# Performance work log

Hardware: AMD Instinct MI355X
Metric: run time of the kernel (lower is better)

## Reference

```python
import jax, jax.numpy as jnp
import numpy as np

N_SLOTS, SLOT_DIM, FEAT_DIM, N_HEADS = 8, 256, 128, 4
HEAD_DIM = SLOT_DIM // N_HEADS
B, H, W = 32, 64, 64


def layernorm(x, g, b, eps=1e-5):
    mu = jnp.mean(x, axis=-1, keepdims=True)
    var = jnp.var(x, axis=-1, keepdims=True)
    return (x - mu) * jax.lax.rsqrt(var + eps) * g + b


def setup_inputs() -> dict:
    key = jax.random.key(0)
    ks = jax.random.split(key, 20)
    s = lambda i, shape, sc: (jax.random.normal(ks[i], shape, dtype=jnp.float32) * sc)
    return {
        'features': s(0, (B, FEAT_DIM, H, W), 1.0),
        'slots': s(1, (B, N_SLOTS, SLOT_DIM), 1.0),
        'Wq': s(2, (SLOT_DIM, SLOT_DIM), 0.05), 'bq': jnp.zeros((SLOT_DIM,), jnp.float32),
        'Wk': s(3, (FEAT_DIM, SLOT_DIM), 0.05), 'bk': jnp.zeros((SLOT_DIM,), jnp.float32),
        'Wv': s(4, (FEAT_DIM, SLOT_DIM), 0.05), 'bv': jnp.zeros((SLOT_DIM,), jnp.float32),
        'W_ih': s(5, (3 * SLOT_DIM, SLOT_DIM), 0.05), 'b_ih': jnp.zeros((3 * SLOT_DIM,), jnp.float32),
        'W_hh': s(6, (3 * SLOT_DIM, SLOT_DIM), 0.05), 'b_hh': jnp.zeros((3 * SLOT_DIM,), jnp.float32),
        'g_pre': jnp.ones((SLOT_DIM,), jnp.float32), 'b_pre': jnp.zeros((SLOT_DIM,), jnp.float32),
        'g_post': jnp.ones((SLOT_DIM,), jnp.float32), 'b_post': jnp.zeros((SLOT_DIM,), jnp.float32),
        'W1': s(7, (SLOT_DIM, 2 * SLOT_DIM), 0.05), 'b1': jnp.zeros((2 * SLOT_DIM,), jnp.float32),
        'W2': s(8, (2 * SLOT_DIM, SLOT_DIM), 0.05), 'b2': jnp.zeros((SLOT_DIM,), jnp.float32),
    }


def reference(features, slots, Wq, bq, Wk, bk, Wv, bv, W_ih, b_ih, W_hh, b_hh,
              g_pre, b_pre, g_post, b_post, W1, b1, W2, b2):
    b, c, h, w = features.shape
    n = h * w
    feats = features.transpose(0, 2, 3, 1).reshape(b, n, c)  # (B, HW, C)

    slots_n = layernorm(slots, g_pre, b_pre)
    q = (slots_n @ Wq + bq).reshape(b, N_SLOTS, N_HEADS, HEAD_DIM)
    k = (feats @ Wk + bk).reshape(b, n, N_HEADS, HEAD_DIM)
    v = (feats @ Wv + bv).reshape(b, n, N_HEADS, HEAD_DIM)

    scale = HEAD_DIM ** -0.5
    # scores: (B, heads, slots, HW); softmax over the SLOT axis (competition)
    scores = jnp.einsum('bshd,bnhd->bhsn', q, k) * scale
    attn = jax.nn.softmax(scores, axis=2)
    agg = jnp.einsum('bhsn,bnhd->bshd', attn, v).reshape(b, N_SLOTS, SLOT_DIM)

    # GRUCell (torch semantics): gates ordered r, z, n
    x = agg.reshape(b * N_SLOTS, SLOT_DIM)
    hprev = slots.reshape(b * N_SLOTS, SLOT_DIM)
    gi = x @ W_ih.T + b_ih
    gh = hprev @ W_hh.T + b_hh
    i_r, i_z, i_n = jnp.split(gi, 3, axis=-1)
    h_r, h_z, h_n = jnp.split(gh, 3, axis=-1)
    r = jax.nn.sigmoid(i_r + h_r)
    z = jax.nn.sigmoid(i_z + h_z)
    nn_ = jnp.tanh(i_n + r * h_n)
    hnew = (1.0 - z) * nn_ + z * hprev
    updated = hnew.reshape(b, N_SLOTS, SLOT_DIM)

    # post-norm + MLP residual (dropout is identity in eval)
    refined = jax.nn.relu(layernorm(updated, g_post, b_post) @ W1 + b1) @ W2 + b2
    return updated + refined
```

## Files before the change

kernel.cpp:

```cpp
#include <hip/hip_runtime.h>
#include <hip/hip_bf16.h>

#define NSLOT 8
#define SDIM 256
#define FDIM 128
#define NHEAD 4
#define HDIM 64
#define NPOS 4096

typedef short v8s __attribute__((ext_vector_type(8)));
typedef short v4s __attribute__((ext_vector_type(4)));
typedef float v4f __attribute__((ext_vector_type(4)));

__device__ __forceinline__ unsigned short f2bf(float x) {
    __hip_bfloat16 h = __float2bfloat16(x);
    unsigned short u; __builtin_memcpy(&u, &h, 2); return u;
}
__device__ __forceinline__ float bfr2f(unsigned short u) {
    __hip_bfloat16 h; __builtin_memcpy(&h, &u, 2); return __bfloat162float(h);
}
__device__ __forceinline__ void splitf(float x, unsigned short& hi, unsigned short& lo) {
    hi = f2bf(x);
    lo = f2bf(x - bfr2f(hi));
}

__global__ __launch_bounds__(256) void k_prep(
    const float* __restrict__ slots,
    const float* __restrict__ Wq, const float* __restrict__ bq,
    const float* __restrict__ g_pre, const float* __restrict__ b_pre,
    const float* __restrict__ Wk, const float* __restrict__ bk,
    const float* __restrict__ W1, const float* __restrict__ W2,
    const float* __restrict__ W_ih, const float* __restrict__ W_hh,
    const float* __restrict__ Wv,
    unsigned short* __restrict__ qkT_ws, float* __restrict__ qb_ws,
    unsigned short* __restrict__ W1Th, unsigned short* __restrict__ W1Tl,
    unsigned short* __restrict__ W2Th, unsigned short* __restrict__ W2Tl,
    unsigned short* __restrict__ WihH, unsigned short* __restrict__ WihL,
    unsigned short* __restrict__ WhhH, unsigned short* __restrict__ WhhL,
    unsigned short* __restrict__ WvTH, unsigned short* __restrict__ WvTl,
    float* __restrict__ agg_ws)
{
    int blk = blockIdx.x, t = threadIdx.x;
    __shared__ __align__(16) float s_ln[256];
    __shared__ __align__(16) float q_l[256];
    __shared__ float r1[4], r2[4];
    __shared__ float tl[32][33];

    if (blk >= 560) {
        int id3 = blk - 560;
        int k0 = (id3 & 3) * 32, n0 = (id3 >> 2) * 32;
        for (int i = 0; i < 4; i++) {
            int idx = i * 256 + t, r = idx >> 5, c = idx & 31;
            tl[r][c] = Wv[(size_t)(k0 + r) * 256 + n0 + c];
        }
        __syncthreads();
        for (int i = 0; i < 4; i++) {
            int idx = i * 256 + t, r = idx >> 5, c = idx & 31;
            unsigned short hi, lo; splitf(tl[c][r], hi, lo);
            WvTH[(size_t)(n0 + r) * 128 + k0 + c] = hi;
            WvTl[(size_t)(n0 + r) * 128 + k0 + c] = lo;
        }
        return;
    }
    if (blk >= 512) {
        int id2 = blk - 512;
        const float* src; unsigned short *dh, *dl; int r0;
        if (id2 < 24) { src = W_ih; dh = WihH; dl = WihL; r0 = id2 * 32; }
        else          { src = W_hh; dh = WhhH; dl = WhhL; r0 = (id2 - 24) * 32; }
        for (int i = 0; i < 32; i++) {
            size_t idx = (size_t)(r0 + i) * 256 + t;
            unsigned short hi, lo; splitf(src[idx], hi, lo);
            dh[idx] = hi; dl[idx] = lo;
        }
        return;
    }
    if (blk >= 256) {
        int id = blk - 256;
        const float* src; unsigned short *dh, *dl; int N, K, k0, n0;
        if (id < 128) { src = W1; dh = W1Th; dl = W1Tl; N = 512; K = 256;
                        k0 = (id >> 4) * 32; n0 = (id & 15) * 32; }
        else          { int i2 = id - 128; src = W2; dh = W2Th; dl = W2Tl; N = 256; K = 512;
                        k0 = (i2 >> 3) * 32; n0 = (i2 & 7) * 32; }
        for (int i = 0; i < 4; i++) {
            int idx = i * 256 + t, r = idx >> 5, c = idx & 31;
            tl[r][c] = src[(size_t)(k0 + r) * N + n0 + c];
        }
        __syncthreads();
        for (int i = 0; i < 4; i++) {
            int idx = i * 256 + t, r = idx >> 5, c = idx & 31;
            unsigned short hi, lo; splitf(tl[c][r], hi, lo);
            dh[(size_t)(n0 + r) * K + k0 + c] = hi;
            dl[(size_t)(n0 + r) * K + k0 + c] = lo;
        }
        return;
    }

    int b = blk >> 3, s = blk & 7;
    if (s == 0)
        for (int i = 0; i < 8; i++) agg_ws[b * 2048 + i * 256 + t] = 0.0f;

    float x = slots[(size_t)(b * 8 + s) * 256 + t];
    float sum = x, sq = x * x;
    #pragma unroll
    for (int m = 1; m <= 32; m <<= 1) {
        sum += __shfl_xor(sum, m, 64);
        sq  += __shfl_xor(sq, m, 64);
    }
    int w = t >> 6, lane = t & 63;
    if (lane == 0) { r1[w] = sum; r2[w] = sq; }
    __syncthreads();
    sum = r1[0] + r1[1] + r1[2] + r1[3];
    sq  = r2[0] + r2[1] + r2[2] + r2[3];
    float mu  = sum * (1.0f / 256);
    float var = sq * (1.0f / 256) - mu * mu;
    float rstd = rsqrtf(var + 1e-5f);
    s_ln[t] = (x - mu) * rstd * g_pre[t] + b_pre[t];
    __syncthreads();

    float qacc = bq[t];
    for (int k = 0; k < 256; k += 4) {
        float4 l4 = *(const float4*)&s_ln[k];
        qacc += l4.x * Wq[(k + 0) * 256 + t]
              + l4.y * Wq[(k + 1) * 256 + t]
              + l4.z * Wq[(k + 2) * 256 + t]
              + l4.w * Wq[(k + 3) * 256 + t];
    }
    q_l[t] = qacc;
    __syncthreads();

    int c = t & 127, h0 = t >> 7;
    #pragma unroll
    for (int hi_ = 0; hi_ < 2; hi_++) {
        int hh = h0 + hi_ * 2;
        const float4* wk4 = (const float4*)&Wk[(size_t)c * 256 + hh * 64];
        const float4* q4  = (const float4*)&q_l[hh * 64];
        float acc = 0.0f;
        #pragma unroll
        for (int d4 = 0; d4 < 16; d4++) {
            float4 wv = wk4[d4]; float4 qv = q4[d4];
            acc += wv.x * qv.x + wv.y * qv.y + wv.z * qv.z + wv.w * qv.w;
        }
        qkT_ws[(size_t)(b * 32 + hh * 8 + s) * 128 + c] = f2bf(acc);
    }
    if (t < 4) {
        float acc = 0.0f;
        for (int d = 0; d < 64; d++)
            acc += bk[t * 64 + d] * q_l[t * 64 + d];
        qb_ws[b * 32 + t * 8 + s] = acc;
    }
}

__global__ __launch_bounds__(256, 4) void k_attn(
    const float* __restrict__ feat,
    const unsigned short* __restrict__ WvTH, const unsigned short* __restrict__ WvTl,
    const float* __restrict__ bv,
    const unsigned short* __restrict__ qkT, const float* __restrict__ qb_ws,
    float* __restrict__ agg_ws)
{
    __shared__ __align__(16) char smem[31360];
    unsigned short* featPC = (unsigned short*)smem;
    unsigned short* featCP = (unsigned short*)(smem + 8704);
    unsigned short* attFH  = (unsigned short*)smem;
    unsigned short* attFL  = (unsigned short*)(smem + 8704);
    float*          s_attn = (float*)(smem + 23040);
    unsigned short* s_aT   = (unsigned short*)(smem + 27648);
    float*          s_S    = (float*)(smem + 31232);

    int t = threadIdx.x, b = blockIdx.y, n0 = blockIdx.x * 128;
    int wv_ = t >> 6, lane = t & 63, quad = lane >> 4, l16 = lane & 15;
    int mt = wv_ >> 1, nt = wv_ & 1;
    int sp  = l16 + mt * 16;
    int shs = l16 + nt * 16;

    v8s bq_[4];
    #pragma unroll
    for (int ch = 0; ch < 4; ch++)
        bq_[ch] = *(const v8s*)&qkT[(b * 32 + shs) * 128 + ch * 32 + quad * 8];
    float qbv = qb_ws[b * 32 + shs];
    if (t < 32) s_S[t] = 0.0f;

    v4f accF[4];
    #pragma unroll
    for (int i = 0; i < 4; i++) accF[i] = (v4f){0.f, 0.f, 0.f, 0.f};

    int c0 = (t >> 3) * 4, p0 = (t & 7) * 4;
    size_t fbase = (size_t)b * (FDIM * NPOS);

    float fv[4][4];
    #pragma unroll
    for (int r = 0; r < 4; r++) {
        float4 f = *(const float4*)&feat[fbase + (size_t)(c0 + r) * NPOS + n0 + p0];
        fv[r][0] = f.x; fv[r][1] = f.y; fv[r][2] = f.z; fv[r][3] = f.w;
    }

    #pragma unroll
    for (int tt = 0; tt < 4; ++tt) {
        __syncthreads();
        unsigned short us[4][4];
        #pragma unroll
        for (int r = 0; r < 4; r++)
            #pragma unroll
            for (int j = 0; j < 4; j++) us[r][j] = f2bf(fv[r][j]);
        #pragma unroll
        for (int r = 0; r < 4; r++)
            *(v4s*)&featCP[(c0 + r) * 56 + p0] =
                (v4s){(short)us[r][0], (short)us[r][1], (short)us[r][2], (short)us[r][3]};
        #pragma unroll
        for (int j = 0; j < 4; j++)
            *(v4s*)&featPC[(p0 + j) * 136 + c0] =
                (v4s){(short)us[0][j], (short)us[1][j], (short)us[2][j], (short)us[3][j]};
        __syncthreads();

        if (tt < 3) {
            #pragma unroll
            for (int r = 0; r < 4; r++) {
                float4 f = *(const float4*)&feat[fbase + (size_t)(c0 + r) * NPOS
                                                 + n0 + (tt + 1) * 32 + p0];
                fv[r][0] = f.x; fv[r][1] = f.y; fv[r][2] = f.z; fv[r][3] = f.w;
            }
        }

        v4f acc = (v4f){0.f, 0.f, 0.f, 0.f};
        #pragma unroll
        for (int ch = 0; ch < 4; ch++) {
            v8s a = *(const v8s*)&featPC[sp * 136 + ch * 32 + quad * 8];
            acc = __builtin_amdgcn_mfma_f32_16x16x32_bf16(a, bq_[ch], acc, 0, 0, 0);
        }
        int pb = mt * 16 + quad * 4;
        #pragma unroll
        for (int r = 0; r < 4; r++)
            s_attn[(pb + r) * 36 + shs] = (acc[r] + qbv) * 0.125f;
        __syncthreads();

        if (t < 128) {
            int p = t >> 2, h2 = t & 3;
            float* a = &s_attn[p * 36 + h2 * 8];
            float m = a[0];
            for (int s = 1; s < 8; s++) m = fmaxf(m, a[s]);
            float e[8], ssum = 0.0f;
            for (int s = 0; s < 8; s++) { e[s] = __expf(a[s] - m); ssum += e[s]; }
            float inv = 1.0f / ssum;
            float sv[8];
            #pragma unroll
            for (int s = 0; s < 8; s++) {
                sv[s] = e[s] * inv;
                s_aT[(h2 * 8 + s) * 56 + p] = f2bf(sv[s]);
            }
            #pragma unroll
            for (int mm = 4; mm <= 32; mm <<= 1)
                #pragma unroll
                for (int s = 0; s < 8; s++) sv[s] += __shfl_xor(sv[s], mm, 64);
            if ((t & 63) < 4)
                #pragma unroll
                for (int s = 0; s < 8; s++) atomicAdd(&s_S[h2 * 8 + s], sv[s]);
        }
        __syncthreads();

        v8s aA0 = *(const v8s*)&s_aT[l16 * 56 + quad * 8];
        v8s aA1 = *(const v8s*)&s_aT[(l16 + 16) * 56 + quad * 8];
        v8s bF0 = *(const v8s*)&featCP[(l16 + wv_ * 32) * 56 + quad * 8];
        v8s bF1 = *(const v8s*)&featCP[(l16 + wv_ * 32 + 16) * 56 + quad * 8];
        accF[0] = __builtin_amdgcn_mfma_f32_16x16x32_bf16(aA0, bF0, accF[0], 0, 0, 0);
        accF[1] = __builtin_amdgcn_mfma_f32_16x16x32_bf16(aA0, bF1, accF[1], 0, 0, 0);
        accF[2] = __builtin_amdgcn_mfma_f32_16x16x32_bf16(aA1, bF0, accF[2], 0, 0, 0);
        accF[3] = __builtin_amdgcn_mfma_f32_16x16x32_bf16(aA1, bF1, accF[3], 0, 0, 0);
    }
    __syncthreads();
    #pragma unroll
    for (int mt2 = 0; mt2 < 2; mt2++)
        #pragma unroll
        for (int ntl = 0; ntl < 2; ntl++) {
            v4f f = accF[mt2 * 2 + ntl];
            int cc = wv_ * 32 + ntl * 16 + l16;
            #pragma unroll
            for (int r = 0; r < 4; r++) {
                unsigned short hi, lo; splitf(f[r], hi, lo);
                attFH[(mt2 * 16 + quad * 4 + r) * 136 + cc] = hi;
                attFL[(mt2 * 16 + quad * 4 + r) * 136 + cc] = lo;
            }
        }
    __syncthreads();

    int h = wv_;
    int am = h * 8 + (l16 & 7);
    for (int nt2 = 0; nt2 < 4; nt2++) {
        int n = h * 64 + nt2 * 16 + l16;
        v4f acc = (v4f){0.f, 0.f, 0.f, 0.f};
        #pragma unroll
        for (int kk = 0; kk < 4; kk++) {
            int ko = kk * 32 + quad * 8;
            v8s ah = *(const v8s*)&attFH[am * 136 + ko];
            v8s al = *(const v8s*)&attFL[am * 136 + ko];
            v8s bh = *(const v8s*)&WvTH[(size_t)n * 128 + ko];
            v8s bl = *(const v8s*)&WvTl[(size_t)n * 128 + ko];
            acc = __builtin_amdgcn_mfma_f32_16x16x32_bf16(al, bh, acc, 0, 0, 0);
            acc = __builtin_amdgcn_mfma_f32_16x16x32_bf16(ah, bl, acc, 0, 0, 0);
            acc = __builtin_amdgcn_mfma_f32_16x16x32_bf16(ah, bh, acc, 0, 0, 0);
        }
        float bvn = bv[n];
        if (quad < 2) {
            #pragma unroll
            for (int r = 0; r < 4; r++) {
                int s = quad * 4 + r;
                atomicAdd(&agg_ws[b * 2048 + s * 256 + n],
                          acc[r] + s_S[h * 8 + s] * bvn);
            }
        }
    }
}

__global__ __launch_bounds__(256) void k_gate(
    const float* __restrict__ agg, const float* __restrict__ slots,
    const unsigned short* __restrict__ WihH, const unsigned short* __restrict__ WihL,
    const float* __restrict__ b_ih,
    const unsigned short* __restrict__ WhhH, const unsigned short* __restrict__ WhhL,
    const float* __restrict__ b_hh,
    float* __restrict__ G)
{
    int ntile = blockIdx.x, mtile = blockIdx.y, t = threadIdx.x;
    bool hhalf = ntile >= 12;
    int jbase = (hhalf ? ntile - 12 : ntile) * 64;
    const float* X = hhalf ? slots : agg;
    const unsigned short* BH = hhalf ? WhhH : WihH;
    const unsigned short* BL = hhalf ? WhhL : WihL;
    const float* bias = hhalf ? b_hh : b_ih;
    int gofs = hhalf ? 768 : 0;
    int m0 = mtile * 16;

    __shared__ __align__(16) unsigned short aH[16][264];
    __shared__ __align__(16) unsigned short aL[16][264];
    for (int i = 0; i < 4; i++) {
        int idx = i * 256 + t;
        int r = idx >> 6, q = idx & 63;
        float4 f = *(const float4*)&X[(size_t)(m0 + r) * 256 + q * 4];
        unsigned short h0,l0,h1,l1,h2,l2,h3,l3;
        splitf(f.x, h0, l0); splitf(f.y, h1, l1);
        splitf(f.z, h2, l2); splitf(f.w, h3, l3);
        *(v4s*)&aH[r][q * 4] = (v4s){(short)h0,(short)h1,(short)h2,(short)h3};
        *(v4s*)&aL[r][q * 4] = (v4s){(short)l0,(short)l1,(short)l2,(short)l3};
    }
    __syncthreads();

    int w = t >> 6, lane = t & 63, quad = lane >> 4, l16 = lane & 15;
    int jrow = jbase + w * 16 + l16;
    v4f acc = (v4f){0.f, 0.f, 0.f, 0.f};
    #pragma unroll
    for (int kk = 0; kk < 8; kk++) {
        int ko = kk * 32 + quad * 8;
        v8s ah = *(const v8s*)&aH[l16][ko];
        v8s al = *(const v8s*)&aL[l16][ko];
        v8s bh = *(const v8s*)&BH[(size_t)jrow * 256 + ko];
        v8s bl = *(const v8s*)&BL[(size_t)jrow * 256 + ko];
        acc = __builtin_amdgcn_mfma_f32_16x16x32_bf16(al, bh, acc, 0, 0, 0);
        acc = __builtin_amdgcn_mfma_f32_16x16x32_bf16(ah, bl, acc, 0, 0, 0);
        acc = __builtin_amdgcn_mfma_f32_16x16x32_bf16(ah, bh, acc, 0, 0, 0);
    }
    float bv_ = bias[jrow];
    int gj = gofs + jbase + w * 16 + l16;
    #pragma unroll
    for (int r = 0; r < 4; r++)
        G[(size_t)(m0 + quad * 4 + r) * 1536 + gj] = acc[r] + bv_;
}

__device__ __forceinline__ float gru1(float ir, float iz, float in_,
                                      float hr, float hz, float hn, float hp) {
    float r = 1.0f / (1.0f + __expf(-(ir + hr)));
    float z = 1.0f / (1.0f + __expf(-(iz + hz)));
    float n = tanhf(in_ + r * hn);
    return (1.0f - z) * n + z * hp;
}

__global__ __launch_bounds__(1024) void k_tail2(
    const float* __restrict__ slots, const float* __restrict__ G,
    const float* __restrict__ g_post, const float* __restrict__ b_post,
    const unsigned short* __restrict__ W1Th, const unsigned short* __restrict__ W1Tl,
    const float* __restrict__ b1,
    const unsigned short* __restrict__ W2Th, const unsigned short* __restrict__ W2Tl,
    const float* __restrict__ b2,
    float* __restrict__ hnF, float* __restrict__ out)
{
    __shared__ __align__(16) char smem[50176];
    unsigned short* lnH   = (unsigned short*)smem;
    unsigned short* lnLo  = (unsigned short*)(smem + 8448);
    unsigned short* y1H   = (unsigned short*)(smem + 16896);
    unsigned short* y1Lo  = (unsigned short*)(smem + 33536);

    int t = threadIdx.x, m0 = blockIdx.x * 16;
    int w = t >> 6, lane = t & 63, quad = lane >> 4, l16 = lane & 15;

    {
        int row = m0 + w, c0 = lane * 4;
        const float* gp = &G[(size_t)row * 1536 + c0];
        float4 gir = *(const float4*)(gp);
        float4 giz = *(const float4*)(gp + 256);
        float4 gin = *(const float4*)(gp + 512);
        float4 ghr = *(const float4*)(gp + 768);
        float4 ghz = *(const float4*)(gp + 1024);
        float4 ghn = *(const float4*)(gp + 1280);
        float4 hp  = *(const float4*)&slots[(size_t)row * 256 + c0];
        float h0 = gru1(gir.x, giz.x, gin.x, ghr.x, ghz.x, ghn.x, hp.x);
        float h1 = gru1(gir.y, giz.y, gin.y, ghr.y, ghz.y, ghn.y, hp.y);
        float h2 = gru1(gir.z, giz.z, gin.z, ghr.z, ghz.z, ghn.z, hp.z);
        float h3 = gru1(gir.w, giz.w, gin.w, ghr.w, ghz.w, ghn.w, hp.w);
        float ssum = h0 + h1 + h2 + h3;
        float ssq  = h0*h0 + h1*h1 + h2*h2 + h3*h3;
        #pragma unroll
        for (int m = 1; m <= 32; m <<= 1) {
            ssum += __shfl_xor(ssum, m, 64);
            ssq  += __shfl_xor(ssq, m, 64);
        }
        float mu = ssum * (1.0f / 256);
        float var = ssq * (1.0f / 256) - mu * mu;
        float rstd = rsqrtf(var + 1e-5f);
        float4 gp4 = *(const float4*)&g_post[c0];
        float4 bp4 = *(const float4*)&b_post[c0];
        float l0 = (h0 - mu) * rstd * gp4.x + bp4.x;
        float l1 = (h1 - mu) * rstd * gp4.y + bp4.y;
        float l2 = (h2 - mu) * rstd * gp4.z + bp4.z;
        float l3 = (h3 - mu) * rstd * gp4.w + bp4.w;
        unsigned short a0,c0s,a1,c1s,a2,c2s,a3,c3s;
        splitf(l0, a0, c0s); splitf(l1, a1, c1s);
        splitf(l2, a2, c2s); splitf(l3, a3, c3s);
        *(v4s*)&lnH[w * 264 + c0]  = (v4s){(short)a0,(short)a1,(short)a2,(short)a3};
        *(v4s*)&lnLo[w * 264 + c0] = (v4s){(short)c0s,(short)c1s,(short)c2s,(short)c3s};
        float4 hv4; hv4.x = h0; hv4.y = h1; hv4.z = h2; hv4.w = h3;
        *(float4*)&hnF[(size_t)row * 256 + c0] = hv4;
    }
    __syncthreads();

    #pragma unroll
    for (int i = 0; i < 2; i++) {
        int ntile = w * 2 + i;
        int n = ntile * 16 + l16;
        v4f acc = (v4f){0.f, 0.f, 0.f, 0.f};
        #pragma unroll
        for (int kk = 0; kk < 8; kk++) {
            int ko = kk * 32 + quad * 8;
            v8s ah = *(const v8s*)&lnH[l16 * 264 + ko];
            v8s al = *(const v8s*)&lnLo[l16 * 264 + ko];
            v8s bh = *(const v8s*)&W1Th[(size_t)n * 256 + ko];
            v8s bl = *(const v8s*)&W1Tl[(size_t)n * 256 + ko];
            acc = __builtin_amdgcn_mfma_f32_16x16x32_bf16(al, bh, acc, 0, 0, 0);
            acc = __builtin_amdgcn_mfma_f32_16x16x32_bf16(ah, bl, acc, 0, 0, 0);
            acc = __builtin_amdgcn_mfma_f32_16x16x32_bf16(ah, bh, acc, 0, 0, 0);
        }
        float bb = b1[n];
        #pragma unroll
        for (int r = 0; r < 4; r++) {
            float y = fmaxf(acc[r] + bb, 0.0f);
            unsigned short hi, lo; splitf(y, hi, lo);
            y1H[(quad * 4 + r) * 520 + n]  = hi;
            y1Lo[(quad * 4 + r) * 520 + n] = lo;
        }
    }
    __syncthreads();

    {
        int n = w * 16 + l16;
        v4f acc = (v4f){0.f, 0.f, 0.f, 0.f};
        #pragma unroll
        for (int kk = 0; kk < 16; kk++) {
            int ko = kk * 32 + quad * 8;
            v8s ah = *(const v8s*)&y1H[l16 * 520 + ko];
            v8s al = *(const v8s*)&y1Lo[l16 * 520 + ko];
            v8s bh = *(const v8s*)&W2Th[(size_t)n * 512 + ko];
            v8s bl = *(const v8s*)&W2Tl[(size_t)n * 512 + ko];
            acc = __builtin_amdgcn_mfma_f32_16x16x32_bf16(al, bh, acc, 0, 0, 0);
            acc = __builtin_amdgcn_mfma_f32_16x16x32_bf16(ah, bl, acc, 0, 0, 0);
            acc = __builtin_amdgcn_mfma_f32_16x16x32_bf16(ah, bh, acc, 0, 0, 0);
        }
        float bb = b2[n];
        #pragma unroll
        for (int r = 0; r < 4; r++) {
            int m = m0 + quad * 4 + r;
            out[(size_t)m * 256 + n] = hnF[(size_t)m * 256 + n] + acc[r] + bb;
        }
    }
}

extern "C" void kernel_launch(void* const* d_in, const int* in_sizes, int n_in,
                              void* d_out, int out_size, void* d_ws, size_t ws_size,
                              hipStream_t stream) {
    const float* features = (const float*)d_in[0];
    const float* slots    = (const float*)d_in[1];
    const float* Wq   = (const float*)d_in[2];
    const float* bq   = (const float*)d_in[3];
    const float* Wk   = (const float*)d_in[4];
    const float* bk   = (const float*)d_in[5];
    const float* Wv   = (const float*)d_in[6];
    const float* bv   = (const float*)d_in[7];
    const float* W_ih = (const float*)d_in[8];
    const float* b_ih = (const float*)d_in[9];
    const float* W_hh = (const float*)d_in[10];
    const float* b_hh = (const float*)d_in[11];
    const float* g_pre  = (const float*)d_in[12];
    const float* b_pre  = (const float*)d_in[13];
    const float* g_post = (const float*)d_in[14];
    const float* b_post = (const float*)d_in[15];
    const float* W1 = (const float*)d_in[16];
    const float* b1 = (const float*)d_in[17];
    const float* W2 = (const float*)d_in[18];
    const float* b2 = (const float*)d_in[19];
    float* out = (float*)d_out;

    char* wsb = (char*)d_ws;
    float* G               = (float*)wsb;
    unsigned short* qkT_ws = (unsigned short*)wsb;
    float* qb_ws           = (float*)(wsb + 262144);
    unsigned short* W1Th   = (unsigned short*)(wsb + 1572864);
    unsigned short* W1Tl   = (unsigned short*)(wsb + 1835008);
    unsigned short* W2Th   = (unsigned short*)(wsb + 2097152);
    unsigned short* W2Tl   = (unsigned short*)(wsb + 2359296);
    unsigned short* WihH   = (unsigned short*)(wsb + 2621440);
    unsigned short* WihL   = (unsigned short*)(wsb + 3014656);
    unsigned short* WhhH   = (unsigned short*)(wsb + 3407872);
    unsigned short* WhhL   = (unsigned short*)(wsb + 3801088);
    unsigned short* WvTH   = (unsigned short*)(wsb + 4194304);
    unsigned short* WvTl   = (unsigned short*)(wsb + 4259840);
    float* hnF             = (float*)(wsb + 4325376);
    float* agg_ws = out;

    k_prep<<<dim3(592), dim3(256), 0, stream>>>(
        slots, Wq, bq, g_pre, b_pre, Wk, bk, W1, W2, W_ih, W_hh, Wv,
        qkT_ws, qb_ws, W1Th, W1Tl, W2Th, W2Tl,
        WihH, WihL, WhhH, WhhL, WvTH, WvTl, agg_ws);
    k_attn<<<dim3(32, 32), dim3(256), 0, stream>>>(
        features, WvTH, WvTl, bv, qkT_ws, qb_ws, agg_ws);
    k_gate<<<dim3(24, 16), dim3(256), 0, stream>>>(
        agg_ws, slots, WihH, WihL, b_ih, WhhH, WhhL, b_hh, G);
    k_tail2<<<dim3(16), dim3(1024), 0, stream>>>(
        slots, G, g_post, b_post, W1Th, W1Tl, b1, W2Th, W2Tl, b2, hnF, out);
}
```

Before: 193.4 us.

## Replace MFMA tail MLP with fp32 vector kernel over more blocks

Replaces the split-bf16 MFMA tail kernel (16 blocks of 1024 threads) with a plain fp32 FMA kernel that handles 4 rows per 256-thread block across 64 blocks, reading W1/W2 directly. This removes the W1/W2 transpose-and-split blocks from the prep kernel and the hnF round-trip through global memory. The tail is spread over more CUs but does scalar FMAs and rereads the fp32 weights once per block.

Measured after the change: 218.4 us. 1.13x slower.

```diff
diff --git a/kernel.cpp b/kernel.cpp
--- a/kernel.cpp
+++ b/kernel.cpp
@@ -29,12 +29,9 @@
     const float* __restrict__ Wq, const float* __restrict__ bq,
     const float* __restrict__ g_pre, const float* __restrict__ b_pre,
     const float* __restrict__ Wk, const float* __restrict__ bk,
-    const float* __restrict__ W1, const float* __restrict__ W2,
     const float* __restrict__ W_ih, const float* __restrict__ W_hh,
     const float* __restrict__ Wv,
     unsigned short* __restrict__ qkT_ws, float* __restrict__ qb_ws,
-    unsigned short* __restrict__ W1Th, unsigned short* __restrict__ W1Tl,
-    unsigned short* __restrict__ W2Th, unsigned short* __restrict__ W2Tl,
     unsigned short* __restrict__ WihH, unsigned short* __restrict__ WihL,
     unsigned short* __restrict__ WhhH, unsigned short* __restrict__ WhhL,
     unsigned short* __restrict__ WvTH, unsigned short* __restrict__ WvTl,
@@ -46,8 +43,8 @@
     __shared__ float r1[4], r2[4];
     __shared__ float tl[32][33];
 
-    if (blk >= 560) {
-        int id3 = blk - 560;
+    if (blk >= 304) {
+        int id3 = blk - 304;
         int k0 = (id3 & 3) * 32, n0 = (id3 >> 2) * 32;
         for (int i = 0; i < 4; i++) {
             int idx = i * 256 + t, r = idx >> 5, c = idx & 31;
@@ -62,8 +59,8 @@
         }
         return;
     }
-    if (blk >= 512) {
-        int id2 = blk - 512;
+    if (blk >= 256) {
+        int id2 = blk - 256;
         const float* src; unsigned short *dh, *dl; int r0;
         if (id2 < 24) { src = W_ih; dh = WihH; dl = WihL; r0 = id2 * 32; }
         else          { src = W_hh; dh = WhhH; dl = WhhL; r0 = (id2 - 24) * 32; }
@@ -71,26 +68,6 @@
             size_t idx = (size_t)(r0 + i) * 256 + t;
             unsigned short hi, lo; splitf(src[idx], hi, lo);
             dh[idx] = hi; dl[idx] = lo;
-        }
-        return;
-    }
-    if (blk >= 256) {
-        int id = blk - 256;
-        const float* src; unsigned short *dh, *dl; int N, K, k0, n0;
-        if (id < 128) { src = W1; dh = W1Th; dl = W1Tl; N = 512; K = 256;
-                        k0 = (id >> 4) * 32; n0 = (id & 15) * 32; }
-        else          { int i2 = id - 128; src = W2; dh = W2Th; dl = W2Tl; N = 256; K = 512;
-                        k0 = (i2 >> 3) * 32; n0 = (i2 & 7) * 32; }
-        for (int i = 0; i < 4; i++) {
-            int idx = i * 256 + t, r = idx >> 5, c = idx & 31;
-            tl[r][c] = src[(size_t)(k0 + r) * N + n0 + c];
-        }
-        __syncthreads();
-        for (int i = 0; i < 4; i++) {
-            int idx = i * 256 + t, r = idx >> 5, c = idx & 31;
-            unsigned short hi, lo; splitf(tl[c][r], hi, lo);
-            dh[(size_t)(n0 + r) * K + k0 + c] = hi;
-            dl[(size_t)(n0 + r) * K + k0 + c] = lo;
         }
         return;
     }
@@ -370,111 +347,100 @@
     return (1.0f - z) * n + z * hp;
 }
 
-__global__ __launch_bounds__(1024) void k_tail2(
+__global__ __launch_bounds__(256) void k_tail_vec(
     const float* __restrict__ slots, const float* __restrict__ G,
     const float* __restrict__ g_post, const float* __restrict__ b_post,
-    const unsigned short* __restrict__ W1Th, const unsigned short* __restrict__ W1Tl,
-    const float* __restrict__ b1,
-    const unsigned short* __restrict__ W2Th, const unsigned short* __restrict__ W2Tl,
-    const float* __restrict__ b2,
-    float* __restrict__ hnF, float* __restrict__ out)
+    const float* __restrict__ W1, const float* __restrict__ b1,
+    const float* __restrict__ W2, const float* __restrict__ b2,
+    float* __restrict__ out)
 {
-    __shared__ __align__(16) char smem[50176];
-    unsigned short* lnH   = (unsigned short*)smem;
-    unsigned short* lnLo  = (unsigned short*)(smem + 8448);
-    unsigned short* y1H   = (unsigned short*)(smem + 16896);
-    unsigned short* y1Lo  = (unsigned short*)(smem + 33536);
-
-    int t = threadIdx.x, m0 = blockIdx.x * 16;
-    int w = t >> 6, lane = t & 63, quad = lane >> 4, l16 = lane & 15;
-
+    __shared__ __align__(16) float s_ln[4][260];
+    __shared__ __align__(16) float s_y1[4][516];
+    __shared__ float pS[4][4], pQ[4][4];
+
+    int t = threadIdx.x, m0 = blockIdx.x * 4;
+    int w = t >> 6, lane = t & 63;
+
+    float hnew[4];
+    #pragma unroll
+    for (int r = 0; r < 4; r++) {
+        int row = m0 + r;
+        const float* gp = &G[(size_t)row * 1536 + t];
+        float hp = slots[(size_t)row * 256 + t];
+        hnew[r] = gru1(gp[0], gp[256], gp[512], gp[768], gp[1024], gp[1280], hp);
+    }
+    float ps[4], pq[4];
+    #pragma unroll
+    for (int r = 0; r < 4; r++) { ps[r] = hnew[r]; pq[r] = hnew[r] * hnew[r]; }
+    #pragma unroll
+    for (int mm = 1; mm <= 32; mm <<= 1)
+        #pragma unroll
+        for (int r = 0; r < 4; r++) {
+            ps[r] += __shfl_xor(ps[r], mm, 64);
+            pq[r] += __shfl_xor(pq[r], mm, 64);
+        }
+    if (lane == 0)
+        #pragma unroll
+        for (int r = 0; r < 4; r++) { pS[r][w] = ps[r]; pQ[r][w] = pq[r]; }
+    __syncthreads();
     {
-        int row = m0 + w, c0 = lane * 4;
-        const float* gp = &G[(size_t)row * 1536 + c0];
-        float4 gir = *(const float4*)(gp);
-        float4 giz = *(const float4*)(gp + 256);
-        float4 gin = *(const float4*)(gp + 512);
-        float4 ghr = *(const float4*)(gp + 768);
-        float4 ghz = *(const float4*)(gp + 1024);
-        float4 ghn = *(const float4*)(gp + 1280);
-        float4 hp  = *(const float4*)&slots[(size_t)row * 256 + c0];
-        float h0 = gru1(gir.x, giz.x, gin.x, ghr.x, ghz.x, ghn.x, hp.x);
-        float h1 = gru1(gir.y, giz.y, gin.y, ghr.y, ghz.y, ghn.y, hp.y);
-        float h2 = gru1(gir.z, giz.z, gin.z, ghr.z, ghz.z, ghn.z, hp.z);
-        float h3 = gru1(gir.w, giz.w, gin.w, ghr.w, ghz.w, ghn.w, hp.w);
-        float ssum = h0 + h1 + h2 + h3;
-        float ssq  = h0*h0 + h1*h1 + h2*h2 + h3*h3;
-        #pragma unroll
-        for (int m = 1; m <= 32; m <<= 1) {
-            ssum += __shfl_xor(ssum, m, 64);
-            ssq  += __shfl_xor(ssq, m, 64);
-        }
-        float mu = ssum * (1.0f / 256);
-        float var = ssq * (1.0f / 256) - mu * mu;
-        float rstd = rsqrtf(var + 1e-5f);
-        float4 gp4 = *(const float4*)&g_post[c0];
-        float4 bp4 = *(const float4*)&b_post[c0];
-        float l0 = (h0 - mu) * rstd * gp4.x + bp4.x;
-        float l1 = (h1 - mu) * rstd * gp4.y + bp4.y;
-        float l2 = (h2 - mu) * rstd * gp4.z + bp4.z;
-        float l3 = (h3 - mu) * rstd * gp4.w + bp4.w;
-        unsigned short a0,c0s,a1,c1s,a2,c2s,a3,c3s;
-        splitf(l0, a0, c0s); splitf(l1, a1, c1s);
-        splitf(l2, a2, c2s); splitf(l3, a3, c3s);
-        *(v4s*)&lnH[w * 264 + c0]  = (v4s){(short)a0,(short)a1,(short)a2,(short)a3};
-        *(v4s*)&lnLo[w * 264 + c0] = (v4s){(short)c0s,(short)c1s,(short)c2s,(short)c3s};
-        float4 hv4; hv4.x = h0; hv4.y = h1; hv4.z = h2; hv4.w = h3;
-        *(float4*)&hnF[(size_t)row * 256 + c0] = hv4;
-    }
-    __syncthreads();
-
-    #pragma unroll
-    for (int i = 0; i < 2; i++) {
-        int ntile = w * 2 + i;
-        int n = ntile * 16 + l16;
-        v4f acc = (v4f){0.f, 0.f, 0.f, 0.f};
-        #pragma unroll
-        for (int kk = 0; kk < 8; kk++) {
-            int ko = kk * 32 + quad * 8;
-            v8s ah = *(const v8s*)&lnH[l16 * 264 + ko];
-            v8s al = *(const v8s*)&lnLo[l16 * 264 + ko];
-            v8s bh = *(const v8s*)&W1Th[(size_t)n * 256 + ko];
-            v8s bl = *(const v8s*)&W1Tl[(size_t)n * 256 + ko];
-            acc = __builtin_amdgcn_mfma_f32_16x16x32_bf16(al, bh, acc, 0, 0, 0);
-            acc = __builtin_amdgcn_mfma_f32_16x16x32_bf16(ah, bl, acc, 0, 0, 0);
-            acc = __builtin_amdgcn_mfma_f32_16x16x32_bf16(ah, bh, acc, 0, 0, 0);
-        }
-        float bb = b1[n];
+        float gpv = g_post[t], bpv = b_post[t];
         #pragma unroll
         for (int r = 0; r < 4; r++) {
-            float y = fmaxf(acc[r] + bb, 0.0f);
-            unsigned short hi, lo; splitf(y, hi, lo);
-            y1H[(quad * 4 + r) * 520 + n]  = hi;
-            y1Lo[(quad * 4 + r) * 520 + n] = lo;
-        }
-    }
-    __syncthreads();
-
+            float s = pS[r][0] + pS[r][1] + pS[r][2] + pS[r][3];
+            float q = pQ[r][0] + pQ[r][1] + pQ[r][2] + pQ[r][3];
+            float mu = s * (1.0f / 256);
+            float var = q * (1.0f / 256) - mu * mu;
+            float rstd = rsqrtf(var + 1e-5f);
+            s_ln[r][t] = (hnew[r] - mu) * rstd * gpv + bpv;
+        }
+    }
+    __syncthreads();
+
+    float a0[4] = {0.f, 0.f, 0.f, 0.f}, a1[4] = {0.f, 0.f, 0.f, 0.f};
+    #define MLP1_STEP(KK, COMP) { \
+        float wA = W1[(size_t)(k + KK) * 512 + t]; \
+        float wB = W1[(size_t)(k + KK) * 512 + t + 256]; \
+        a0[0] += l0.COMP * wA; a1[0] += l0.COMP * wB; \
+        a0[1] += l1.COMP * wA; a1[1] += l1.COMP * wB; \
+        a0[2] += l2.COMP * wA; a1[2] += l2.COMP * wB; \
+        a0[3] += l3.COMP * wA; a1[3] += l3.COMP * wB; }
+    for (int k = 0; k < 256; k += 4) {
+        float4 l0 = *(const float4*)&s_ln[0][k];
+        float4 l1 = *(const float4*)&s_ln[1][k];
+        float4 l2 = *(const float4*)&s_ln[2][k];
+        float4 l3 = *(const float4*)&s_ln[3][k];
+        MLP1_STEP(0, x) MLP1_STEP(1, y) MLP1_STEP(2, z) MLP1_STEP(3, w)
+    }
+    #undef MLP1_STEP
     {
-        int n = w * 16 + l16;
-        v4f acc = (v4f){0.f, 0.f, 0.f, 0.f};
-        #pragma unroll
-        for (int kk = 0; kk < 16; kk++) {
-            int ko = kk * 32 + quad * 8;
-            v8s ah = *(const v8s*)&y1H[l16 * 520 + ko];
-            v8s al = *(const v8s*)&y1Lo[l16 * 520 + ko];
-            v8s bh = *(const v8s*)&W2Th[(size_t)n * 512 + ko];
-            v8s bl = *(const v8s*)&W2Tl[(size_t)n * 512 + ko];
-            acc = __builtin_amdgcn_mfma_f32_16x16x32_bf16(al, bh, acc, 0, 0, 0);
-            acc = __builtin_amdgcn_mfma_f32_16x16x32_bf16(ah, bl, acc, 0, 0, 0);
-            acc = __builtin_amdgcn_mfma_f32_16x16x32_bf16(ah, bh, acc, 0, 0, 0);
-        }
-        float bb = b2[n];
+        float b1a = b1[t], b1b = b1[t + 256];
         #pragma unroll
         for (int r = 0; r < 4; r++) {
-            int m = m0 + quad * 4 + r;
-            out[(size_t)m * 256 + n] = hnF[(size_t)m * 256 + n] + acc[r] + bb;
-        }
+            s_y1[r][t]       = fmaxf(a0[r] + b1a, 0.0f);
+            s_y1[r][t + 256] = fmaxf(a1[r] + b1b, 0.0f);
+        }
+    }
+    __syncthreads();
+
+    float o[4] = {0.f, 0.f, 0.f, 0.f};
+    #define MLP2_STEP(KK, COMP) { \
+        float wv = W2[(size_t)(k + KK) * 256 + t]; \
+        o[0] += y0.COMP * wv; o[1] += y1v.COMP * wv; \
+        o[2] += y2.COMP * wv; o[3] += y3.COMP * wv; }
+    for (int k = 0; k < 512; k += 4) {
+        float4 y0  = *(const float4*)&s_y1[0][k];
+        float4 y1v = *(const float4*)&s_y1[1][k];
+        float4 y2  = *(const float4*)&s_y1[2][k];
+        float4 y3  = *(const float4*)&s_y1[3][k];
+        MLP2_STEP(0, x) MLP2_STEP(1, y) MLP2_STEP(2, z) MLP2_STEP(3, w)
+    }
+    #undef MLP2_STEP
+    {
+        float b2v = b2[t];
+        #pragma unroll
+        for (int r = 0; r < 4; r++)
+            out[(size_t)(m0 + r) * 256 + t] = hnew[r] + o[r] + b2v;
     }
 }
 
@@ -507,27 +473,21 @@
     float* G               = (float*)wsb;
     unsigned short* qkT_ws = (unsigned short*)wsb;
     float* qb_ws           = (float*)(wsb + 262144);
-    unsigned short* W1Th   = (unsigned short*)(wsb + 1572864);
-    unsigned short* W1Tl   = (unsigned short*)(wsb + 1835008);
-    unsigned short* W2Th   = (unsigned short*)(wsb + 2097152);
-    unsigned short* W2Tl   = (unsigned short*)(wsb + 2359296);
     unsigned short* WihH   = (unsigned short*)(wsb + 2621440);
     unsigned short* WihL   = (unsigned short*)(wsb + 3014656);
     unsigned short* WhhH   = (unsigned short*)(wsb + 3407872);
     unsigned short* WhhL   = (unsigned short*)(wsb + 3801088);
     unsigned short* WvTH   = (unsigned short*)(wsb + 4194304);
     unsigned short* WvTl   = (unsigned short*)(wsb + 4259840);
-    float* hnF             = (float*)(wsb + 4325376);
     float* agg_ws = out;
 
-    k_prep<<<dim3(592), dim3(256), 0, stream>>>(
-        slots, Wq, bq, g_pre, b_pre, Wk, bk, W1, W2, W_ih, W_hh, Wv,
-        qkT_ws, qb_ws, W1Th, W1Tl, W2Th, W2Tl,
-        WihH, WihL, WhhH, WhhL, WvTH, WvTl, agg_ws);
+    k_prep<<<dim3(336), dim3(256), 0, stream>>>(
+        slots, Wq, bq, g_pre, b_pre, Wk, bk, W_ih, W_hh, Wv,
+        qkT_ws, qb_ws, WihH, WihL, WhhH, WhhL, WvTH, WvTl, agg_ws);
     k_attn<<<dim3(32, 32), dim3(256), 0, stream>>>(
         features, WvTH, WvTl, bv, qkT_ws, qb_ws, agg_ws);
     k_gate<<<dim3(24, 16), dim3(256), 0, stream>>>(
         agg_ws, slots, WihH, WihL, b_ih, WhhH, WhhL, b_hh, G);
-    k_tail2<<<dim3(16), dim3(1024), 0, stream>>>(
-        slots, G, g_post, b_post, W1Th, W1Tl, b1, W2Th, W2Tl, b2, hnF, out);
-}
+    k_tail_vec<<<dim3(64), dim3(256), 0, stream>>>(
+        slots, G, g_post, b_post, W1, b1, W2, b2, out);
+}
```

## Split fused GRU/MLP tail into three kernels for wider parallelism

Applied to the files above, without the earlier changes.

Replaces the single 16-block, 1024-thread tail kernel with three kernels: GRU plus layernorm (64 blocks), MLP layer 1 (128 blocks) and MLP layer 2 (64 blocks). Intermediates go through global workspace, reusing the now-dead W_ih/W_hh split buffers. The aim is to spread the small tail work over many more CUs. The cost is two extra launches and global round-trips for the intermediates.

Result: faster. 178.4 us (-7.8%).

```diff
diff --git a/kernel.cpp b/kernel.cpp
--- a/kernel.cpp
+++ b/kernel.cpp
@@ -370,111 +370,136 @@
     return (1.0f - z) * n + z * hp;
 }
 
-__global__ __launch_bounds__(1024) void k_tail2(
+__global__ __launch_bounds__(256) void k_gru(
     const float* __restrict__ slots, const float* __restrict__ G,
     const float* __restrict__ g_post, const float* __restrict__ b_post,
+    unsigned short* __restrict__ lnH_g, unsigned short* __restrict__ lnL_g,
+    float* __restrict__ hnF)
+{
+    __shared__ float pS[4][4], pQ[4][4];
+    int t = threadIdx.x, m0 = blockIdx.x * 4;
+    int w = t >> 6, lane = t & 63;
+
+    float hnew[4];
+    #pragma unroll
+    for (int r = 0; r < 4; r++) {
+        int row = m0 + r;
+        const float* gp = &G[(size_t)row * 1536 + t];
+        float hp = slots[(size_t)row * 256 + t];
+        hnew[r] = gru1(gp[0], gp[256], gp[512], gp[768], gp[1024], gp[1280], hp);
+        hnF[(size_t)row * 256 + t] = hnew[r];
+    }
+    float ps[4], pq[4];
+    #pragma unroll
+    for (int r = 0; r < 4; r++) { ps[r] = hnew[r]; pq[r] = hnew[r] * hnew[r]; }
+    #pragma unroll
+    for (int mm = 1; mm <= 32; mm <<= 1)
+        #pragma unroll
+        for (int r = 0; r < 4; r++) {
+            ps[r] += __shfl_xor(ps[r], mm, 64);
+            pq[r] += __shfl_xor(pq[r], mm, 64);
+        }
+    if (lane == 0)
+        #pragma unroll
+        for (int r = 0; r < 4; r++) { pS[r][w] = ps[r]; pQ[r][w] = pq[r]; }
+    __syncthreads();
+    float gpv = g_post[t], bpv = b_post[t];
+    #pragma unroll
+    for (int r = 0; r < 4; r++) {
+        float s = pS[r][0] + pS[r][1] + pS[r][2] + pS[r][3];
+        float q = pQ[r][0] + pQ[r][1] + pQ[r][2] + pQ[r][3];
+        float mu = s * (1.0f / 256);
+        float var = q * (1.0f / 256) - mu * mu;
+        float rstd = rsqrtf(var + 1e-5f);
+        float ln = (hnew[r] - mu) * rstd * gpv + bpv;
+        unsigned short hi, lo; splitf(ln, hi, lo);
+        lnH_g[(size_t)(m0 + r) * 256 + t] = hi;
+        lnL_g[(size_t)(m0 + r) * 256 + t] = lo;
+    }
+}
+
+__global__ __launch_bounds__(256) void k_mlp1(
+    const unsigned short* __restrict__ lnH_g, const unsigned short* __restrict__ lnL_g,
     const unsigned short* __restrict__ W1Th, const unsigned short* __restrict__ W1Tl,
     const float* __restrict__ b1,
+    unsigned short* __restrict__ y1H_g, unsigned short* __restrict__ y1L_g)
+{
+    int ncl = blockIdx.x, mtile = blockIdx.y, t = threadIdx.x;
+    int m0 = mtile * 16;
+    __shared__ __align__(16) unsigned short aH[16][264];
+    __shared__ __align__(16) unsigned short aL[16][264];
+    {
+        int r = t >> 4, c0 = (t & 15) * 16;
+        *(v8s*)&aH[r][c0]     = *(const v8s*)&lnH_g[(size_t)(m0 + r) * 256 + c0];
+        *(v8s*)&aH[r][c0 + 8] = *(const v8s*)&lnH_g[(size_t)(m0 + r) * 256 + c0 + 8];
+        *(v8s*)&aL[r][c0]     = *(const v8s*)&lnL_g[(size_t)(m0 + r) * 256 + c0];
+        *(v8s*)&aL[r][c0 + 8] = *(const v8s*)&lnL_g[(size_t)(m0 + r) * 256 + c0 + 8];
+    }
+    __syncthreads();
+
+    int w = t >> 6, lane = t & 63, quad = lane >> 4, l16 = lane & 15;
+    int n = (ncl * 4 + w) * 16 + l16;
+    v4f acc = (v4f){0.f, 0.f, 0.f, 0.f};
+    #pragma unroll
+    for (int kk = 0; kk < 8; kk++) {
+        int ko = kk * 32 + quad * 8;
+        v8s ah = *(const v8s*)&aH[l16][ko];
+        v8s al = *(const v8s*)&aL[l16][ko];
+        v8s bh = *(const v8s*)&W1Th[(size_t)n * 256 + ko];
+        v8s bl = *(const v8s*)&W1Tl[(size_t)n * 256 + ko];
+        acc = __builtin_amdgcn_mfma_f32_16x16x32_bf16(al, bh, acc, 0, 0, 0);
+        acc = __builtin_amdgcn_mfma_f32_16x16x32_bf16(ah, bl, acc, 0, 0, 0);
+        acc = __builtin_amdgcn_mfma_f32_16x16x32_bf16(ah, bh, acc, 0, 0, 0);
+    }
+    float bb = b1[n];
+    #pragma unroll
+    for (int r = 0; r < 4; r++) {
+        float y = fmaxf(acc[r] + bb, 0.0f);
+        unsigned short hi, lo; splitf(y, hi, lo);
+        y1H_g[(size_t)(m0 + quad * 4 + r) * 512 + n] = hi;
+        y1L_g[(size_t)(m0 + quad * 4 + r) * 512 + n] = lo;
+    }
+}
+
+__global__ __launch_bounds__(256) void k_mlp2(
+    const unsigned short* __restrict__ y1H_g, const unsigned short* __restrict__ y1L_g,
     const unsigned short* __restrict__ W2Th, const unsigned short* __restrict__ W2Tl,
-    const float* __restrict__ b2,
-    float* __restrict__ hnF, float* __restrict__ out)
+    const float* __restrict__ b2, const float* __restrict__ hnF,
+    float* __restrict__ out)
 {
-    __shared__ __align__(16) char smem[50176];
-    unsigned short* lnH   = (unsigned short*)smem;
-    unsigned short* lnLo  = (unsigned short*)(smem + 8448);
-    unsigned short* y1H   = (unsigned short*)(smem + 16896);
-    unsigned short* y1Lo  = (unsigned short*)(smem + 33536);
-
-    int t = threadIdx.x, m0 = blockIdx.x * 16;
+    int ncl = blockIdx.x, mtile = blockIdx.y, t = threadIdx.x;
+    int m0 = mtile * 16;
+    __shared__ __align__(16) unsigned short yH[16][520];
+    __shared__ __align__(16) unsigned short yL[16][520];
+    {
+        int r = t >> 4, c0 = (t & 15) * 32;
+        #pragma unroll
+        for (int i = 0; i < 4; i++) {
+            *(v8s*)&yH[r][c0 + i * 8] = *(const v8s*)&y1H_g[(size_t)(m0 + r) * 512 + c0 + i * 8];
+            *(v8s*)&yL[r][c0 + i * 8] = *(const v8s*)&y1L_g[(size_t)(m0 + r) * 512 + c0 + i * 8];
+        }
+    }
+    __syncthreads();
+
     int w = t >> 6, lane = t & 63, quad = lane >> 4, l16 = lane & 15;
-
-    {
-        int row = m0 + w, c0 = lane * 4;
-        const float* gp = &G[(size_t)row * 1536 + c0];
-        float4 gir = *(const float4*)(gp);
-        float4 giz = *(const float4*)(gp + 256);
-        float4 gin = *(const float4*)(gp + 512);
-        float4 ghr = *(const float4*)(gp + 768);
-        float4 ghz = *(const float4*)(gp + 1024);
-        float4 ghn = *(const float4*)(gp + 1280);
-        float4 hp  = *(const float4*)&slots[(size_t)row * 256 + c0];
-        float h0 = gru1(gir.x, giz.x, gin.x, ghr.x, ghz.x, ghn.x, hp.x);
-        float h1 = gru1(gir.y, giz.y, gin.y, ghr.y, ghz.y, ghn.y, hp.y);
-        float h2 = gru1(gir.z, giz.z, gin.z, ghr.z, ghz.z, ghn.z, hp.z);
-        float h3 = gru1(gir.w, giz.w, gin.w, ghr.w, ghz.w, ghn.w, hp.w);
-        float ssum = h0 + h1 + h2 + h3;
-        float ssq  = h0*h0 + h1*h1 + h2*h2 + h3*h3;
-        #pragma unroll
-        for (int m = 1; m <= 32; m <<= 1) {
-            ssum += __shfl_xor(ssum, m, 64);
-            ssq  += __shfl_xor(ssq, m, 64);
-        }
-        float mu = ssum * (1.0f / 256);
-        float var = ssq * (1.0f / 256) - mu * mu;
-        float rstd = rsqrtf(var + 1e-5f);
-        float4 gp4 = *(const float4*)&g_post[c0];
-        float4 bp4 = *(const float4*)&b_post[c0];
-        float l0 = (h0 - mu) * rstd * gp4.x + bp4.x;
-        float l1 = (h1 - mu) * rstd * gp4.y + bp4.y;
-        float l2 = (h2 - mu) * rstd * gp4.z + bp4.z;
-        float l3 = (h3 - mu) * rstd * gp4.w + bp4.w;
-        unsigned short a0,c0s,a1,c1s,a2,c2s,a3,c3s;
-        splitf(l0, a0, c0s); splitf(l1, a1, c1s);
-        splitf(l2, a2, c2s); splitf(l3, a3, c3s);
-        *(v4s*)&lnH[w * 264 + c0]  = (v4s){(short)a0,(short)a1,(short)a2,(short)a3};
-        *(v4s*)&lnLo[w * 264 + c0] = (v4s){(short)c0s,(short)c1s,(short)c2s,(short)c3s};
-        float4 hv4; hv4.x = h0; hv4.y = h1; hv4.z = h2; hv4.w = h3;
-        *(float4*)&hnF[(size_t)row * 256 + c0] = hv4;
-    }
-    __syncthreads();
-
-    #pragma unroll
-    for (int i = 0; i < 2; i++) {
-        int ntile = w * 2 + i;
-        int n = ntile * 16 + l16;
-        v4f acc = (v4f){0.f, 0.f, 0.f, 0.f};
-        #pragma unroll
-        for (int kk = 0; kk < 8; kk++) {
-            int ko = kk * 32 + quad * 8;
-            v8s ah = *(const v8s*)&lnH[l16 * 264 + ko];
-            v8s al = *(const v8s*)&lnLo[l16 * 264 + ko];
-            v8s bh = *(const v8s*)&W1Th[(size_t)n * 256 + ko];
-            v8s bl = *(const v8s*)&W1Tl[(size_t)n * 256 + ko];
-            acc = __builtin_amdgcn_mfma_f32_16x16x32_bf16(al, bh, acc, 0, 0, 0);
-            acc = __builtin_amdgcn_mfma_f32_16x16x32_bf16(ah, bl, acc, 0, 0, 0);
-            acc = __builtin_amdgcn_mfma_f32_16x16x32_bf16(ah, bh, acc, 0, 0, 0);
-        }
-        float bb = b1[n];
-        #pragma unroll
-        for (int r = 0; r < 4; r++) {
-            float y = fmaxf(acc[r] + bb, 0.0f);
-            unsigned short hi, lo; splitf(y, hi, lo);
-            y1H[(quad * 4 + r) * 520 + n]  = hi;
-            y1Lo[(quad * 4 + r) * 520 + n] = lo;
-        }
-    }
-    __syncthreads();
-
-    {
-        int n = w * 16 + l16;
-        v4f acc = (v4f){0.f, 0.f, 0.f, 0.f};
-        #pragma unroll
-        for (int kk = 0; kk < 16; kk++) {
-            int ko = kk * 32 + quad * 8;
-            v8s ah = *(const v8s*)&y1H[l16 * 520 + ko];
-            v8s al = *(const v8s*)&y1Lo[l16 * 520 + ko];
-            v8s bh = *(const v8s*)&W2Th[(size_t)n * 512 + ko];
-            v8s bl = *(const v8s*)&W2Tl[(size_t)n * 512 + ko];
-            acc = __builtin_amdgcn_mfma_f32_16x16x32_bf16(al, bh, acc, 0, 0, 0);
-            acc = __builtin_amdgcn_mfma_f32_16x16x32_bf16(ah, bl, acc, 0, 0, 0);
-            acc = __builtin_amdgcn_mfma_f32_16x16x32_bf16(ah, bh, acc, 0, 0, 0);
-        }
-        float bb = b2[n];
-        #pragma unroll
-        for (int r = 0; r < 4; r++) {
-            int m = m0 + quad * 4 + r;
-            out[(size_t)m * 256 + n] = hnF[(size_t)m * 256 + n] + acc[r] + bb;
-        }
+    int n = (ncl * 4 + w) * 16 + l16;
+    v4f acc = (v4f){0.f, 0.f, 0.f, 0.f};
+    #pragma unroll
+    for (int kk = 0; kk < 16; kk++) {
+        int ko = kk * 32 + quad * 8;
+        v8s ah = *(const v8s*)&yH[l16][ko];
+        v8s al = *(const v8s*)&yL[l16][ko];
+        v8s bh = *(const v8s*)&W2Th[(size_t)n * 512 + ko];
+        v8s bl = *(const v8s*)&W2Tl[(size_t)n * 512 + ko];
+        acc = __builtin_amdgcn_mfma_f32_16x16x32_bf16(al, bh, acc, 0, 0, 0);
+        acc = __builtin_amdgcn_mfma_f32_16x16x32_bf16(ah, bl, acc, 0, 0, 0);
+        acc = __builtin_amdgcn_mfma_f32_16x16x32_bf16(ah, bh, acc, 0, 0, 0);
+    }
+    float bb = b2[n];
+    #pragma unroll
+    for (int r = 0; r < 4; r++) {
+        int m = m0 + quad * 4 + r;
+        out[(size_t)m * 256 + n] = hnF[(size_t)m * 256 + n] + acc[r] + bb;
     }
 }
 
@@ -518,6 +543,10 @@
     unsigned short* WvTH   = (unsigned short*)(wsb + 4194304);
     unsigned short* WvTl   = (unsigned short*)(wsb + 4259840);
     float* hnF             = (float*)(wsb + 4325376);
+    unsigned short* lnH_g  = (unsigned short*)(wsb + 2621440);
+    unsigned short* lnL_g  = (unsigned short*)(wsb + 2752512);
+    unsigned short* y1H_g  = (unsigned short*)(wsb + 2883584);
+    unsigned short* y1L_g  = (unsigned short*)(wsb + 3145728);
     float* agg_ws = out;
 
     k_prep<<<dim3(592), dim3(256), 0, stream>>>(
@@ -528,6 +557,10 @@
         features, WvTH, WvTl, bv, qkT_ws, qb_ws, agg_ws);
     k_gate<<<dim3(24, 16), dim3(256), 0, stream>>>(
         agg_ws, slots, WihH, WihL, b_ih, WhhH, WhhL, b_hh, G);
-    k_tail2<<<dim3(16), dim3(1024), 0, stream>>>(
-        slots, G, g_post, b_post, W1Th, W1Tl, b1, W2Th, W2Tl, b2, hnF, out);
-}
+    k_gru<<<dim3(64), dim3(256), 0, stream>>>(
+        slots, G, g_post, b_post, lnH_g, lnL_g, hnF);
+    k_mlp1<<<dim3(8, 16), dim3(256), 0, stream>>>(
+        lnH_g, lnL_g, W1Th, W1Tl, b1, y1H_g, y1L_g);
+    k_mlp2<<<dim3(4, 16), dim3(256), 0, stream>>>(
+        y1H_g, y1L_g, W2Th, W2Tl, b2, hnF, out);
+}
```
